# Optimization experiments

Measured on AMD Instinct MI355X. Metric: run time of the kernel, lower is better.

The kernel has to match this reference:

```python
import jax, jax.numpy as jnp
import numpy as np

V, B, C, NS, H, W = 3, 2, 64, 32, 128, 128


def setup_inputs() -> dict:
    key = jax.random.key(0)
    k1, k2 = jax.random.split(key, 2)
    features = jax.random.normal(k1, (V, B, C, H, W), dtype=jnp.float32)
    f = 1.1 * W
    K = np.array([[f, 0.0, (W - 1) / 2.0],
                  [0.0, f, (H - 1) / 2.0],
                  [0.0, 0.0, 1.0]], dtype=np.float32)
    intrinsics = jnp.asarray(np.broadcast_to(K, (V, B, 3, 3)).copy())
    c2w = np.tile(np.eye(4, dtype=np.float32), (V, B, 1, 1))
    rng = np.random.default_rng(0)
    for v in range(1, V):
        for b in range(B):
            th = rng.uniform(-0.03, 0.03)
            Ry = np.array([[np.cos(th), 0.0, np.sin(th)],
                           [0.0, 1.0, 0.0],
                           [-np.sin(th), 0.0, np.cos(th)]], dtype=np.float32)
            c2w[v, b, :3, :3] = Ry
            c2w[v, b, :3, 3] = rng.uniform(-0.1, 0.1, size=3).astype(np.float32)
    cam_to_world = jnp.asarray(c2w)
    scale_hypo = jnp.broadcast_to(jnp.linspace(0.5, 1.5, NS, dtype=jnp.float32), (B, NS)) + jnp.zeros((B, NS), jnp.float32)
    depth_init = 2.0 + 4.0 * jax.random.uniform(k2, (B, H, W), dtype=jnp.float32)
    return {"features": features, "intrinsics": intrinsics, "cam_to_world": cam_to_world,
            "scale_hypo": scale_hypo, "depth_init": depth_init}


def _grid_sample_zeros(feat, grid):
    """torch F.grid_sample(mode='bilinear', padding_mode='zeros', align_corners=False)."""
    Bn, Cn, Hn, Wn = feat.shape
    ix = ((grid[..., 0] + 1.0) * Wn - 1.0) * 0.5
    iy = ((grid[..., 1] + 1.0) * Hn - 1.0) * 0.5
    x0 = jnp.floor(ix); y0 = jnp.floor(iy)
    x1 = x0 + 1.0; y1 = y0 + 1.0
    wx1 = ix - x0; wx0 = 1.0 - wx1
    wy1 = iy - y0; wy0 = 1.0 - wy1
    featf = feat.reshape(Bn, Cn, Hn * Wn)

    def corner(xc, yc, w):
        valid = (xc >= 0) & (xc <= Wn - 1) & (yc >= 0) & (yc <= Hn - 1)
        xi = jnp.clip(xc, 0, Wn - 1).astype(jnp.int32)
        yi = jnp.clip(yc, 0, Hn - 1).astype(jnp.int32)
        idx = (yi * Wn + xi).reshape(Bn, 1, -1)
        v = jnp.take_along_axis(featf, idx, axis=2)  # (B,C,Npts)
        return v * (w * valid).reshape(Bn, 1, -1)

    out = (corner(x0, y0, wx0 * wy0) + corner(x1, y0, wx1 * wy0)
           + corner(x0, y1, wx0 * wy1) + corner(x1, y1, wx1 * wy1))
    return out.reshape(Bn, Cn, grid.shape[1], grid.shape[2])


def _homo_warp(src_feat, scale_hypo, depth_init, src_K, src_c2w, ref_K, ref_c2w):
    # src_feat (B,C,H,W); depth_init (B,1,H,W); returns (B,C,Ns,H,W)
    Bn, Cn, Hn, Wn = src_feat.shape
    Ns = scale_hypo.shape[1]

    def build_grid():
        src_w2c = jnp.linalg.inv(src_c2w)
        ref_w2c = jnp.linalg.inv(ref_c2w)
        # original clones world_to_cam and only replaces the top-left 3x3 with K,
        # so the w2c translation column is kept inside the 'intrinsics' matrix
        src_P = src_w2c.at[:, :3, :3].set(src_K)
        ref_P = ref_w2c.at[:, :3, :3].set(ref_K)
        proj = (src_P @ src_w2c) @ jnp.linalg.inv(ref_P @ ref_w2c)
        rot = proj[:, :3, :3]
        trans = proj[:, :3, 3]
        depth = depth_init.reshape(Bn, 1, 1, Hn * Wn) * scale_hypo[:, None, :, None]  # (B,1,Ns,HW)
        # NOTE: original builds both grid axes from arange(height); valid since H==W
        y, x = jnp.meshgrid(jnp.arange(Hn, dtype=jnp.float32),
                            jnp.arange(Wn, dtype=jnp.float32), indexing='ij')
        xyz = jnp.stack([x.ravel(), y.ravel(), jnp.ones(Hn * Wn, dtype=jnp.float32)])  # (3,HW)
        rot_xyz = jnp.einsum('bij,jn->bin', rot, xyz)                         # (B,3,HW)
        proj_xyz = rot_xyz[:, :, None, :] * depth + trans[:, :, None, None]   # (B,3,Ns,HW)
        proj_xy = proj_xyz[:, :2] / proj_xyz[:, 2:3]
        gx = proj_xy[:, 0] / ((Wn - 1) / 2.0) - 1.0
        gy = proj_xy[:, 1] / ((Hn - 1) / 2.0) - 1.0
        return jnp.stack([gx, gy], axis=-1).reshape(Bn, Ns * Hn, Wn, 2)

    grid = jax.lax.stop_gradient(build_grid())  # torch computes the grid under no_grad
    warped = _grid_sample_zeros(src_feat, grid)
    return warped.reshape(Bn, Cn, Ns, Hn, Wn)


def reference(features, intrinsics, cam_to_world, scale_hypo, depth_init):
    num_views = features.shape[0]
    Bn, Cn, Hn, Wn = features.shape[1:]
    Ns = scale_hypo.shape[1]
    ref_K, ref_c2w = intrinsics[0], cam_to_world[0]
    # faithfully replicate torch's in-place ref_volume.sub_() bug:
    # ref accumulates the subtraction of every previously-warped volume
    ref_running = jnp.broadcast_to(features[0][:, :, None], (Bn, Cn, Ns, Hn, Wn))
    cost = jnp.zeros((Bn, Ns, Hn, Wn), dtype=features.dtype)
    for v in range(1, num_views):
        warped = _homo_warp(features[v], scale_hypo, depth_init[:, None],
                            intrinsics[v], cam_to_world[v], ref_K, ref_c2w)
        ref_running = ref_running - warped
        cost = cost + jnp.sqrt(jnp.sum(ref_running * ref_running, axis=1))  # L2 over C
    cost = cost / (num_views - 1)
    cost = jnp.mean(cost, axis=(2, 3))          # (B, Nscale)
    prob = jax.nn.softmax(cost, axis=1)
    return jnp.sum(prob * scale_hypo, axis=1)   # (B,)
```

## Files before the change

kernel.cpp:

```cpp
#include <hip/hip_runtime.h>
#include <math.h>

constexpr int NV = 3;
constexpr int NB = 2;
constexpr int NC = 64;
constexpr int NSC = 32;
constexpr int NH = 128;
constexpr int NW = 128;
constexpr int NSB = 4;

typedef _Float16 h2_t __attribute__((ext_vector_type(2)));

template <int CTRL>
__device__ __forceinline__ float dpp_add(float x) {
    int s = __builtin_amdgcn_update_dpp(0, __float_as_int(x), CTRL, 0xf, 0xf, true);
    return x + __int_as_float(s);
}

__device__ __forceinline__ float dot2acc(h2_t a, float acc) {
#if __has_builtin(__builtin_amdgcn_fdot2)
    return __builtin_amdgcn_fdot2(a, a, acc, false);
#else
    float x = (float)a.x, y = (float)a.y;
    return acc + x * x + y * y;
#endif
}

__device__ void inv4x4(const double* m, double* out) {
    double inv[16];
    inv[0]  =  m[5]*m[10]*m[15] - m[5]*m[11]*m[14] - m[9]*m[6]*m[15] + m[9]*m[7]*m[14] + m[13]*m[6]*m[11] - m[13]*m[7]*m[10];
    inv[4]  = -m[4]*m[10]*m[15] + m[4]*m[11]*m[14] + m[8]*m[6]*m[15] - m[8]*m[7]*m[14] - m[12]*m[6]*m[11] + m[12]*m[7]*m[10];
    inv[8]  =  m[4]*m[9]*m[15]  - m[4]*m[11]*m[13] - m[8]*m[5]*m[15] + m[8]*m[7]*m[13] + m[12]*m[5]*m[11] - m[12]*m[7]*m[9];
    inv[12] = -m[4]*m[9]*m[14]  + m[4]*m[10]*m[13] + m[8]*m[5]*m[14] - m[8]*m[6]*m[13] - m[12]*m[5]*m[10] + m[12]*m[6]*m[9];
    inv[1]  = -m[1]*m[10]*m[15] + m[1]*m[11]*m[14] + m[9]*m[2]*m[15] - m[9]*m[3]*m[14] - m[13]*m[2]*m[11] + m[13]*m[3]*m[10];
    inv[5]  =  m[0]*m[10]*m[15] - m[0]*m[11]*m[14] - m[8]*m[2]*m[15] + m[8]*m[3]*m[14] + m[12]*m[2]*m[11] - m[12]*m[3]*m[10];
    inv[9]  = -m[0]*m[9]*m[15]  + m[0]*m[11]*m[13] + m[8]*m[1]*m[15] - m[8]*m[3]*m[13] - m[12]*m[1]*m[11] + m[12]*m[3]*m[9];
    inv[13] =  m[0]*m[9]*m[14]  - m[0]*m[10]*m[13] - m[8]*m[1]*m[14] + m[8]*m[2]*m[13] + m[12]*m[1]*m[10] - m[12]*m[2]*m[9];
    inv[2]  =  m[1]*m[6]*m[15]  - m[1]*m[7]*m[14]  - m[5]*m[2]*m[15] + m[5]*m[3]*m[14] + m[13]*m[2]*m[7]  - m[13]*m[3]*m[6];
    inv[6]  = -m[0]*m[6]*m[15]  + m[0]*m[7]*m[14]  + m[4]*m[2]*m[15] - m[4]*m[3]*m[14] - m[12]*m[2]*m[7]  + m[12]*m[3]*m[6];
    inv[10] =  m[0]*m[5]*m[15]  - m[0]*m[7]*m[13]  - m[4]*m[1]*m[15] + m[4]*m[3]*m[13] + m[12]*m[1]*m[7]  - m[12]*m[3]*m[5];
    inv[14] = -m[0]*m[5]*m[14]  + m[0]*m[6]*m[13]  + m[4]*m[1]*m[14] - m[4]*m[2]*m[13] - m[12]*m[1]*m[6]  + m[12]*m[2]*m[5];
    inv[3]  = -m[1]*m[6]*m[11]  + m[1]*m[7]*m[10]  + m[5]*m[2]*m[11] - m[5]*m[3]*m[10] - m[9]*m[2]*m[7]   + m[9]*m[3]*m[6];
    inv[7]  =  m[0]*m[6]*m[11]  - m[0]*m[7]*m[10]  - m[4]*m[2]*m[11] + m[4]*m[3]*m[10] + m[8]*m[2]*m[7]   - m[8]*m[3]*m[6];
    inv[11] = -m[0]*m[5]*m[11]  + m[0]*m[7]*m[9]   + m[4]*m[1]*m[11] - m[4]*m[3]*m[9]  - m[8]*m[1]*m[7]   + m[8]*m[3]*m[5];
    inv[15] =  m[0]*m[5]*m[10]  - m[0]*m[6]*m[9]   - m[4]*m[1]*m[10] + m[4]*m[2]*m[9]  + m[8]*m[1]*m[6]   - m[8]*m[2]*m[5];
    double det = m[0]*inv[0] + m[1]*inv[4] + m[2]*inv[8] + m[3]*inv[12];
    det = 1.0 / det;
    for (int i = 0; i < 16; ++i) out[i] = inv[i] * det;
}

__device__ void mat4mul(const double* a, const double* b, double* o) {
    for (int i = 0; i < 4; ++i)
        for (int j = 0; j < 4; ++j) {
            double s = 0.0;
            for (int k = 0; k < 4; ++k) s += a[i*4+k] * b[k*4+j];
            o[i*4+j] = s;
        }
}

__global__ __launch_bounds__(256) void transpose_kernel(const float* __restrict__ in,
                                                        unsigned int* __restrict__ out,
                                                        const float* __restrict__ intr,
                                                        const float* __restrict__ c2w,
                                                        float* __restrict__ rt,
                                                        float* __restrict__ cost) {
    __shared__ float tile[NC][NW + 1];
    const int y  = blockIdx.x;
    const int vb = blockIdx.y;

    for (int i = threadIdx.x; i < NC * NW; i += 256) {
        int c = i >> 7;
        int x = i & (NW - 1);
        tile[c][x] = in[((size_t)(vb * NC + c) * NH + y) * NW + x];
    }
    __syncthreads();
    unsigned int* dst = out + ((size_t)vb * NH + y) * NW * (NC / 2);
    for (int i = threadIdx.x; i < NW * (NC / 2); i += 256) {
        int x  = i >> 5;
        int cp = i & 31;
        h2_t h = { (_Float16)tile[2 * cp][x], (_Float16)tile[2 * cp + 1][x] };
        dst[x * (NC / 2) + cp] = __builtin_bit_cast(unsigned int, h);
    }

    if (blockIdx.x == 0 && blockIdx.y == 0) {
        int t = threadIdx.x;
        if (t >= 4 && t < 4 + NB * NSC) cost[t - 4] = 0.f;
        if (t < 2 * NB) {
            int vi = t >> 1;
            int b  = t & 1;
            int v  = vi + 1;

            double src_c2w[16], ref_c2w[16];
            for (int i = 0; i < 16; ++i) {
                src_c2w[i] = (double)c2w[(v * NB + b) * 16 + i];
                ref_c2w[i] = (double)c2w[(0 * NB + b) * 16 + i];
            }
            double src_w2c[16], ref_w2c[16];
            inv4x4(src_c2w, src_w2c);
            inv4x4(ref_c2w, ref_w2c);

            double srcP[16], refP[16];
            for (int i = 0; i < 16; ++i) { srcP[i] = src_w2c[i]; refP[i] = ref_w2c[i]; }
            for (int r = 0; r < 3; ++r)
                for (int c = 0; c < 3; ++c) {
                    srcP[r*4+c] = (double)intr[(v * NB + b) * 9 + r*3 + c];
                    refP[r*4+c] = (double)intr[(0 * NB + b) * 9 + r*3 + c];
                }

            double M1[16], M2[16], M2inv[16];
            mat4mul(srcP, src_w2c, M1);
            mat4mul(refP, ref_w2c, M2);
            inv4x4(M2, M2inv);
            double proj[16];
            mat4mul(M1, M2inv, proj);

            float* o = rt + (vi * NB + b) * 12;
            o[0] = (float)proj[0];  o[1] = (float)proj[1];  o[2]  = (float)proj[2];
            o[3] = (float)proj[4];  o[4] = (float)proj[5];  o[5]  = (float)proj[6];
            o[6] = (float)proj[8];  o[7] = (float)proj[9];  o[8]  = (float)proj[10];
            o[9] = (float)proj[3];  o[10] = (float)proj[7]; o[11] = (float)proj[11];
        }
    }
}

__global__ __launch_bounds__(256) void cost_kernel(
    const unsigned int* __restrict__ ftb,
    const float* __restrict__ depth,
    const float* __restrict__ scale,
    const float* __restrict__ rt,
    float* __restrict__ cost)
{
    const int tid  = threadIdx.x;
    const int lane = tid & 63;
    const int wv   = tid >> 6;
    const int grp  = lane >> 3;
    const int gl   = lane & 7;
    const int nsg  = blockIdx.y;
    const int b    = blockIdx.z;

    const int p = blockIdx.x * 32 + wv * 8 + grp;
    const int x = p & (NW - 1);
    const int y = p >> 7;
    const float fx = (float)x;
    const float fy = (float)y;

    const float d0 = depth[(b * NH + y) * NW + x];

    const uint4* f0q = (const uint4*)(ftb) + ((size_t)(0 * NB + b) * NH * NW + p) * 8 + gl;
    const uint4* v1q = (const uint4*)(ftb) + ((size_t)(1 * NB + b) * NH * NW) * 8 + gl;
    const uint4* v2q = (const uint4*)(ftb) + ((size_t)(2 * NB + b) * NH * NW) * 8 + gl;

    const uint4 f0u = *f0q;
    const h2_t* f0h = (const h2_t*)&f0u;

    float R0[12], R1[12];
#pragma unroll
    for (int k = 0; k < 12; ++k) {
        R0[k] = rt[(0 * NB + b) * 12 + k];
        R1[k] = rt[(1 * NB + b) * 12 + k];
    }
    const float ax0 = R0[0] * fx + R0[1] * fy + R0[2];
    const float ay0 = R0[3] * fx + R0[4] * fy + R0[5];
    const float az0 = R0[6] * fx + R0[7] * fy + R0[8];
    const float ax1 = R1[0] * fx + R1[1] * fy + R1[2];
    const float ay1 = R1[3] * fx + R1[4] * fy + R1[5];
    const float az1 = R1[6] * fx + R1[7] * fy + R1[8];

    const float CXY = 64.0f / 63.5f;

    __shared__ float red[4][NSB];
    float outv[NSB];

#pragma unroll
    for (int nsub = 0; nsub < NSB; ++nsub) {
        const float s = scale[b * NSC + nsg * NSB + nsub];
        const float d = d0 * s;

        int   ti[2][4];
        float tw[2][4];
#pragma unroll
        for (int vi = 0; vi < 2; ++vi) {
            float px = (vi ? ax1 : ax0) * d + (vi ? R1[9]  : R0[9]);
            float py = (vi ? ay1 : ay0) * d + (vi ? R1[10] : R0[10]);
            float pz = (vi ? az1 : az0) * d + (vi ? R1[11] : R0[11]);
            float invz = __builtin_amdgcn_rcpf(pz);
            float ix = (px * invz) * CXY - 0.5f;
            float iy = (py * invz) * CXY - 0.5f;

            float x0f = floorf(ix), y0f = floorf(iy);
            float wx1 = ix - x0f, wx0 = 1.f - wx1;
            float wy1 = iy - y0f, wy0 = 1.f - wy1;

            float mx0 = (x0f >= 0.f  && x0f <= 127.f) ? wx0 : 0.f;
            float mx1 = (x0f >= -1.f && x0f <= 126.f) ? wx1 : 0.f;
            float my0 = (y0f >= 0.f  && y0f <= 127.f) ? wy0 : 0.f;
            float my1 = (y0f >= -1.f && y0f <= 126.f) ? wy1 : 0.f;

            int xi0 = (int)fminf(fmaxf(x0f, 0.f), 127.f);
            int yi0 = (int)fminf(fmaxf(y0f, 0.f), 127.f);
            int xo = (x0f >= 0.f && x0f <= 126.f) ? 8 : 0;
            int yo = (y0f >= 0.f && y0f <= 126.f) ? NW * 8 : 0;

            int base = (yi0 * NW + xi0) * 8;
            ti[vi][0] = base;
            ti[vi][1] = base + xo;
            ti[vi][2] = base + yo;
            ti[vi][3] = base + yo + xo;
            tw[vi][0] = mx0 * my0;
            tw[vi][1] = mx1 * my0;
            tw[vi][2] = mx0 * my1;
            tw[vi][3] = mx1 * my1;
        }

        uint4 t0 = v1q[ti[0][0]];
        uint4 t1 = v1q[ti[0][1]];
        uint4 t2 = v1q[ti[0][2]];
        uint4 t3 = v1q[ti[0][3]];
        uint4 u0 = v2q[ti[1][0]];
        uint4 u1 = v2q[ti[1][1]];
        uint4 u2 = v2q[ti[1][2]];
        uint4 u3 = v2q[ti[1][3]];

        _Float16 w00 = (_Float16)(-tw[0][0]), w01 = (_Float16)(-tw[0][1]);
        _Float16 w02 = (_Float16)(-tw[0][2]), w03 = (_Float16)(-tw[0][3]);
        _Float16 w10 = (_Float16)(-tw[1][0]), w11 = (_Float16)(-tw[1][1]);
        _Float16 w12 = (_Float16)(-tw[1][2]), w13 = (_Float16)(-tw[1][3]);
        h2_t h00 = {w00, w00}, h01 = {w01, w01}, h02 = {w02, w02}, h03 = {w03, w03};
        h2_t h10 = {w10, w10}, h11 = {w11, w11}, h12 = {w12, w12}, h13 = {w13, w13};

        const h2_t* p0 = (const h2_t*)&t0;
        const h2_t* p1 = (const h2_t*)&t1;
        const h2_t* p2 = (const h2_t*)&t2;
        const h2_t* p3 = (const h2_t*)&t3;
        const h2_t* q0 = (const h2_t*)&u0;
        const h2_t* q1 = (const h2_t*)&u1;
        const h2_t* q2 = (const h2_t*)&u2;
        const h2_t* q3 = (const h2_t*)&u3;

        h2_t r[4];
        float sq1 = 0.f, sq2 = 0.f;
#pragma unroll
        for (int j = 0; j < 4; ++j) {
            h2_t rr = f0h[j];
            rr += p0[j] * h00;
            rr += p1[j] * h01;
            rr += p2[j] * h02;
            rr += p3[j] * h03;
            r[j] = rr;
            sq1 = dot2acc(rr, sq1);
        }
#pragma unroll
        for (int j = 0; j < 4; ++j) {
            h2_t rr = r[j];
            rr += q0[j] * h10;
            rr += q1[j] * h11;
            rr += q2[j] * h12;
            rr += q3[j] * h13;
            sq2 = dot2acc(rr, sq2);
        }

        sq1 = dpp_add<0x111>(sq1);
        sq1 = dpp_add<0x112>(sq1);
        sq1 = dpp_add<0x114>(sq1);
        sq2 = dpp_add<0x111>(sq2);
        sq2 = dpp_add<0x112>(sq2);
        sq2 = dpp_add<0x114>(sq2);
        float sv = sqrtf(sq1) + sqrtf(sq2);
        sv = dpp_add<0x118>(sv);
        sv = dpp_add<0x142>(sv);
        sv = dpp_add<0x143>(sv);
        outv[nsub] = sv;
    }

    if (lane == 63) {
#pragma unroll
        for (int nsub = 0; nsub < NSB; ++nsub) red[wv][nsub] = outv[nsub];
    }
    __syncthreads();
    if (tid < NSB) {
        float t = red[0][tid] + red[1][tid] + red[2][tid] + red[3][tid];
        atomicAdd(&cost[b * NSC + nsg * NSB + tid], t * (0.5f / (float)(NH * NW)));
    }
}

__global__ void finalize_kernel(const float* __restrict__ cost,
                                const float* __restrict__ scale,
                                float* __restrict__ out) {
    int tid = threadIdx.x;
    if (tid >= NB * NSC) return;
    int b = tid >> 5;
    int ns = tid & 31;
    float c = cost[b * NSC + ns];
    float sv = scale[b * NSC + ns];

    float m = c;
#pragma unroll
    for (int mk = 1; mk < 32; mk <<= 1) m = fmaxf(m, __shfl_xor(m, mk, 64));
    float e = __expf(c - m);
    float sum = e;
#pragma unroll
    for (int mk = 1; mk < 32; mk <<= 1) sum += __shfl_xor(sum, mk, 64);
    float val = (e / sum) * sv;
#pragma unroll
    for (int mk = 1; mk < 32; mk <<= 1) val += __shfl_xor(val, mk, 64);
    if (ns == 0) out[b] = val;
}

extern "C" void kernel_launch(void* const* d_in, const int* in_sizes, int n_in,
                              void* d_out, int out_size, void* d_ws, size_t ws_size,
                              hipStream_t stream) {
    const float* features   = (const float*)d_in[0];
    const float* intrinsics = (const float*)d_in[1];
    const float* cam2world  = (const float*)d_in[2];
    const float* scale_hypo = (const float*)d_in[3];
    const float* depth_init = (const float*)d_in[4];
    float* out = (float*)d_out;

    unsigned int* ftb = (unsigned int*)d_ws;
    float* rt   = (float*)(ftb + (size_t)NV * NB * NH * NW * (NC / 2));
    float* cost = rt + 2 * NB * 12;

    dim3 tgrid(NH, NV * NB);
    transpose_kernel<<<tgrid, 256, 0, stream>>>(features, ftb, intrinsics, cam2world, rt, cost);

    dim3 cgrid(NH * NW / 32, NSC / NSB, NB);
    cost_kernel<<<cgrid, 256, 0, stream>>>(ftb, depth_init, scale_hypo, rt, cost);

    finalize_kernel<<<1, 64, 0, stream>>>(cost, scale_hypo, out);
}
```

Measured before the change: 166.0 us.

## Fuse softmax finalize into cost kernel via last-block counter; raise scales per block

The separate finalize kernel is removed. A global atomic counter, reset in the transpose kernel, lets the last cost block to finish compute the softmax over scales and the weighted sum. The scales handled per block rise from 4 to 16 with partial unrolling, so the per-pixel setup and feature loads are reused across more hypotheses and fewer blocks issue atomics. The cost is fewer blocks (less parallelism), extra fences and a serial tail in the last block.

Measured after the change: 156.6 us. 1.06x faster.

```diff
diff --git a/kernel.cpp b/kernel.cpp
--- a/kernel.cpp
+++ b/kernel.cpp
@@ -7,7 +7,7 @@
 constexpr int NSC = 32;
 constexpr int NH = 128;
 constexpr int NW = 128;
-constexpr int NSB = 4;
+constexpr int NSB = 16;
 
 typedef _Float16 h2_t __attribute__((ext_vector_type(2)));
 
@@ -63,7 +63,8 @@
                                                         const float* __restrict__ intr,
                                                         const float* __restrict__ c2w,
                                                         float* __restrict__ rt,
-                                                        float* __restrict__ cost) {
+                                                        float* __restrict__ cost,
+                                                        unsigned int* __restrict__ counter) {
     __shared__ float tile[NC][NW + 1];
     const int y  = blockIdx.x;
     const int vb = blockIdx.y;
@@ -85,6 +86,7 @@
     if (blockIdx.x == 0 && blockIdx.y == 0) {
         int t = threadIdx.x;
         if (t >= 4 && t < 4 + NB * NSC) cost[t - 4] = 0.f;
+        if (t == 4 + NB * NSC) *counter = 0u;
         if (t < 2 * NB) {
             int vi = t >> 1;
             int b  = t & 1;
@@ -128,7 +130,10 @@
     const float* __restrict__ depth,
     const float* __restrict__ scale,
     const float* __restrict__ rt,
-    float* __restrict__ cost)
+    float* __restrict__ cost,
+    unsigned int* __restrict__ counter,
+    float* __restrict__ outp,
+    int total_blocks)
 {
     const int tid  = threadIdx.x;
     const int lane = tid & 63;
@@ -169,9 +174,8 @@
     const float CXY = 64.0f / 63.5f;
 
     __shared__ float red[4][NSB];
-    float outv[NSB];
-
-#pragma unroll
+
+#pragma unroll 4
     for (int nsub = 0; nsub < NSB; ++nsub) {
         const float s = scale[b * NSC + nsg * NSB + nsub];
         const float d = d0 * s;
@@ -269,41 +273,42 @@
         sv = dpp_add<0x118>(sv);
         sv = dpp_add<0x142>(sv);
         sv = dpp_add<0x143>(sv);
-        outv[nsub] = sv;
-    }
-
-    if (lane == 63) {
-#pragma unroll
-        for (int nsub = 0; nsub < NSB; ++nsub) red[wv][nsub] = outv[nsub];
-    }
+        if (lane == 63) red[wv][nsub] = sv;
+    }
+
     __syncthreads();
     if (tid < NSB) {
         float t = red[0][tid] + red[1][tid] + red[2][tid] + red[3][tid];
         atomicAdd(&cost[b * NSC + nsg * NSB + tid], t * (0.5f / (float)(NH * NW)));
-    }
-}
-
-__global__ void finalize_kernel(const float* __restrict__ cost,
-                                const float* __restrict__ scale,
-                                float* __restrict__ out) {
-    int tid = threadIdx.x;
-    if (tid >= NB * NSC) return;
-    int b = tid >> 5;
-    int ns = tid & 31;
-    float c = cost[b * NSC + ns];
-    float sv = scale[b * NSC + ns];
-
-    float m = c;
-#pragma unroll
-    for (int mk = 1; mk < 32; mk <<= 1) m = fmaxf(m, __shfl_xor(m, mk, 64));
-    float e = __expf(c - m);
-    float sum = e;
-#pragma unroll
-    for (int mk = 1; mk < 32; mk <<= 1) sum += __shfl_xor(sum, mk, 64);
-    float val = (e / sum) * sv;
-#pragma unroll
-    for (int mk = 1; mk < 32; mk <<= 1) val += __shfl_xor(val, mk, 64);
-    if (ns == 0) out[b] = val;
+        __threadfence();
+    }
+    __syncthreads();
+
+    __shared__ unsigned int lastflag;
+    if (tid == 0) {
+        unsigned int prev = atomicAdd(counter, 1u);
+        lastflag = (prev == (unsigned int)(total_blocks - 1)) ? 1u : 0u;
+    }
+    __syncthreads();
+    if (lastflag && tid < NB * NSC) {
+        __threadfence();
+        int bb = tid >> 5;
+        int ns = tid & 31;
+        float c  = atomicAdd(&cost[bb * NSC + ns], 0.0f);
+        float sv = scale[bb * NSC + ns];
+
+        float m = c;
+#pragma unroll
+        for (int mk = 1; mk < 32; mk <<= 1) m = fmaxf(m, __shfl_xor(m, mk, 64));
+        float e = __expf(c - m);
+        float sum = e;
+#pragma unroll
+        for (int mk = 1; mk < 32; mk <<= 1) sum += __shfl_xor(sum, mk, 64);
+        float val = (e / sum) * sv;
+#pragma unroll
+        for (int mk = 1; mk < 32; mk <<= 1) val += __shfl_xor(val, mk, 64);
+        if (ns == 0) outp[bb] = val;
+    }
 }
 
 extern "C" void kernel_launch(void* const* d_in, const int* in_sizes, int n_in,
@@ -319,12 +324,14 @@
     unsigned int* ftb = (unsigned int*)d_ws;
     float* rt   = (float*)(ftb + (size_t)NV * NB * NH * NW * (NC / 2));
     float* cost = rt + 2 * NB * 12;
+    unsigned int* counter = (unsigned int*)(cost + NB * NSC);
 
     dim3 tgrid(NH, NV * NB);
-    transpose_kernel<<<tgrid, 256, 0, stream>>>(features, ftb, intrinsics, cam2world, rt, cost);
+    transpose_kernel<<<tgrid, 256, 0, stream>>>(features, ftb, intrinsics, cam2world,
+                                                rt, cost, counter);
 
     dim3 cgrid(NH * NW / 32, NSC / NSB, NB);
-    cost_kernel<<<cgrid, 256, 0, stream>>>(ftb, depth_init, scale_hypo, rt, cost);
-
-    finalize_kernel<<<1, 64, 0, stream>>>(cost, scale_hypo, out);
-}
+    int total_blocks = cgrid.x * cgrid.y * cgrid.z;
+    cost_kernel<<<cgrid, 256, 0, stream>>>(ftb, depth_init, scale_hypo, rt,
+                                           cost, counter, out, total_blocks);
+}
```
